# Optimization experiments

Measured on AMD Instinct MI355X. Metric: run time of the kernel, lower is better.

## Reference

```python
import jax, jax.numpy as jnp
import numpy as np
from jax import lax

B, CIN, COUT, K, H, W, SDIM = 16, 256, 256, 3, 64, 64, 512


def setup_inputs() -> dict:
    key = jax.random.key(0)
    k1, k2, k3, k4 = jax.random.split(key, 4)
    return {
        "x": jax.random.normal(k1, (B, CIN, H, W), jnp.float32),
        "style": jax.random.normal(k2, (B, SDIM), jnp.float32),
        "weight": jax.random.normal(k3, (COUT, CIN, K, K), jnp.float32),
        "style_w": jax.random.normal(k4, (SDIM, CIN), jnp.float32) * (1.0 / np.sqrt(SDIM)),
        "style_b": jnp.zeros((CIN,), jnp.float32),
    }


def reference(x, style, weight, style_w, style_b):
    b, cin, h, w_sz = x.shape
    cout, _, k, _ = weight.shape
    mod_scale = 1.0 / np.sqrt(cin * k * k)
    # style projection: [B, CIN]
    s = style @ style_w + style_b
    # modulate: [B, COUT, CIN, K, K]
    wmod = weight[None] * s[:, None, :, None, None] * mod_scale
    # demodulate over (cin, kh, kw)
    demod = lax.rsqrt(jnp.sum(wmod * wmod, axis=(2, 3, 4)) + 1e-8)  # [B, COUT]
    wmod = wmod * demod[:, :, None, None, None]
    # per-sample conv (groups=batch equivalent) via vmap
    def conv1(xb, wb):
        # xb: [CIN, H, W], wb: [COUT, CIN, K, K]
        return lax.conv_general_dilated(
            xb[None], wb, window_strides=(1, 1), padding=[(1, 1), (1, 1)],
            dimension_numbers=("NCHW", "OIHW", "NCHW"))[0]
    return jax.vmap(conv1)(x, wmod)  # [B, COUT, H, W]
```

## Files before the change

kernel.cpp:

```cpp
#include <hip/hip_runtime.h>
#include <hip/hip_bf16.h>

#define BB 16
#define CIN 256
#define COUT 256
#define HH 64
#define WW 64
#define SDIM 512

typedef __attribute__((ext_vector_type(8))) short bf16x8;
typedef __attribute__((ext_vector_type(4))) float f32x4;

static __device__ __forceinline__ short f2bf(float v) {
    __hip_bfloat16 h = __float2bfloat16(v);
    return *reinterpret_cast<short*>(&h);
}

__global__ void style_proj_kernel(const float* __restrict__ style,
                                  const float* __restrict__ style_w,
                                  const float* __restrict__ style_b,
                                  float* __restrict__ s) {
    __shared__ float red[3][64];
    int l    = threadIdx.x & 63;
    int part = threadIdx.x >> 6;
    int ci   = blockIdx.x * 64 + l;
    int b    = blockIdx.y;
    float acc = 0.f;
    const float* st = style + b * SDIM + part * (SDIM / 4);
    const float* W  = style_w + (size_t)(part * (SDIM / 4)) * CIN + ci;
#pragma unroll 4
    for (int k = 0; k < SDIM / 4; ++k) acc += st[k] * W[(size_t)k * CIN];
    if (part) red[part - 1][l] = acc;
    __syncthreads();
    if (part == 0)
        s[b * CIN + ci] = acc + red[0][l] + red[1][l] + red[2][l] + style_b[ci];
}

__global__ void wprep_kernel(const float* __restrict__ w,
                             __hip_bfloat16* __restrict__ wT,
                             float* __restrict__ wsq) {
    int co = blockIdx.x;
    int ci = threadIdx.x;
    const float* wp = w + ((size_t)co * CIN + ci) * 9;
    float acc = 0.f;
#pragma unroll
    for (int k = 0; k < 9; ++k) {
        float v = wp[k];
        acc += v * v;
        wT[((size_t)co * 9 + k) * CIN + ci] = __float2bfloat16(v);
    }
    wsq[co * CIN + ci] = acc;
}

__global__ void demod_kernel(const float* __restrict__ wsq,
                             const float* __restrict__ s,
                             float* __restrict__ demod) {
    int b    = blockIdx.y;
    int co   = blockIdx.x * 4 + (threadIdx.x >> 6);
    int lane = threadIdx.x & 63;
    float acc = 0.f;
#pragma unroll
    for (int j = 0; j < CIN / 64; ++j) {
        int ci = j * 64 + lane;
        float sv = s[b * CIN + ci];
        acc += wsq[co * CIN + ci] * sv * sv;
    }
#pragma unroll
    for (int off = 32; off > 0; off >>= 1)
        acc += __shfl_down(acc, off, 64);
    if (lane == 0)
        demod[b * COUT + co] = rsqrtf(acc * (1.0f / (CIN * 9)) + 1e-8f);
}

__global__ void xmod_kernel(const float* __restrict__ x,
                            const float* __restrict__ s,
                            __hip_bfloat16* __restrict__ xm) {
    int px = threadIdx.x & 63;
    int y  = blockIdx.x * 4 + (threadIdx.x >> 6);
    int g  = blockIdx.y;
    int b  = blockIdx.z;
    const float* xp = x + (((size_t)(b * CIN + g * 8)) * HH + y) * WW + px;
    const float4* sp = (const float4*)(s + b * CIN + g * 8);
    float4 s0 = sp[0], s1 = sp[1];
    float sv[8] = {s0.x, s0.y, s0.z, s0.w, s1.x, s1.y, s1.z, s1.w};
    bf16x8 v;
#pragma unroll
    for (int c = 0; c < 8; ++c) v[c] = f2bf(xp[(size_t)c * (HH * WW)] * sv[c]);
    *(bf16x8*)(xm + ((((size_t)(b * 32 + g)) * HH + y) * WW + px) * 8) = v;
}

__device__ __forceinline__ void stage_lds(__hip_bfloat16* xsb,
                                          const __hip_bfloat16* __restrict__ xm,
                                          int b, int cc, int Y0, int lane,
                                          int wave) {
#pragma unroll
    for (int i = 0; i < 6; ++i) {
        int u = wave * 6 + i;
        int r = u >> 2, quad = u & 3;
        int y = Y0 - 1 + r;
        if ((unsigned)y < (unsigned)HH) {
            __hip_bfloat16* dst = xsb + (((r * 4 + quad) * 66) + 1) * 8;
            const __hip_bfloat16* src =
                xm + ((((size_t)(b * 32 + cc * 4 + quad)) * HH + y) * WW + lane) * 8;
            __builtin_amdgcn_global_load_lds(
                (const __attribute__((address_space(1))) void*)src,
                (__attribute__((address_space(3))) void*)dst, 16, 0, 0);
        }
    }
}

__global__ __launch_bounds__(256, 3) void conv_mfma_kernel(
    const __hip_bfloat16* __restrict__ xm, const __hip_bfloat16* __restrict__ wT,
    const float* __restrict__ demod, float* __restrict__ out) {
    __shared__ __hip_bfloat16 xs[2][6 * 4 * 66 * 8];

    int tid  = threadIdx.x;
    int lane = tid & 63;
    int wave = tid >> 6;
    int wco  = wave >> 1;
    int rp   = wave & 1;
    int n    = lane & 15;
    int quad = lane >> 4;

    int Y0  = blockIdx.x * 4;
    int co0 = blockIdx.y * 64;
    int b   = blockIdx.z;

    const bf16x8 zv = (bf16x8){0, 0, 0, 0, 0, 0, 0, 0};
    if (tid < 96) {
        int buf = tid / 48, idx = tid % 48;
        int rowq = idx >> 1, col = (idx & 1) * 65;
        *(bf16x8*)(&xs[buf][(rowq * 66 + col) * 8]) = zv;
    }
    if (Y0 == 0) {
        for (int c = tid; c < 528; c += 256) {
            int buf = c / 264, idx = c % 264;
            *(bf16x8*)(&xs[buf][idx * 8]) = zv;
        }
    }
    if (Y0 + 4 == HH) {
        for (int c = tid; c < 528; c += 256) {
            int buf = c / 264, idx = c % 264;
            *(bf16x8*)(&xs[buf][(20 * 66 + idx) * 8]) = zv;
        }
    }

    f32x4 acc[2][2][4];
#pragma unroll
    for (int wr = 0; wr < 2; ++wr)
#pragma unroll
        for (int m = 0; m < 2; ++m)
#pragma unroll
            for (int j = 0; j < 4; ++j) acc[wr][m][j] = (f32x4){0.f, 0.f, 0.f, 0.f};

    const __hip_bfloat16* wb =
        wT + ((size_t)(co0 + wco * 32 + n) * 9) * CIN + quad * 8;

    stage_lds(xs[0], xm, b, 0, Y0, lane, wave);
    __syncthreads();

    for (int cc = 0; cc < 8; ++cc) {
        int cur = cc & 1;

        bf16x8 af[2][9];
#pragma unroll
        for (int k = 0; k < 9; ++k) {
            af[0][k] = *(const bf16x8*)(wb + ((size_t)k) * CIN + cc * 32);
            af[1][k] = *(const bf16x8*)(wb + ((size_t)(16 * 9 + k)) * CIN + cc * 32);
        }
        if (cc < 7) stage_lds(xs[cur ^ 1], xm, b, cc + 1, Y0, lane, wave);

        const __hip_bfloat16* xb = xs[cur];
#pragma unroll
        for (int r4 = 0; r4 < 4; ++r4) {
            int rr = rp * 2 + r4;
#pragma unroll
            for (int dx = 0; dx < 3; ++dx) {
#pragma unroll
                for (int j = 0; j < 4; ++j) {
                    bf16x8 bv = *(const bf16x8*)(
                        xb + (((rr * 4 + quad) * 66) + j * 16 + n + dx) * 8);
                    if (r4 <= 2) {
                        acc[0][0][j] = __builtin_amdgcn_mfma_f32_16x16x32_bf16(
                            af[0][r4 * 3 + dx], bv, acc[0][0][j], 0, 0, 0);
                        acc[0][1][j] = __builtin_amdgcn_mfma_f32_16x16x32_bf16(
                            af[1][r4 * 3 + dx], bv, acc[0][1][j], 0, 0, 0);
                    }
                    if (r4 >= 1) {
                        acc[1][0][j] = __builtin_amdgcn_mfma_f32_16x16x32_bf16(
                            af[0][(r4 - 1) * 3 + dx], bv, acc[1][0][j], 0, 0, 0);
                        acc[1][1][j] = __builtin_amdgcn_mfma_f32_16x16x32_bf16(
                            af[1][(r4 - 1) * 3 + dx], bv, acc[1][1][j], 0, 0, 0);
                    }
                }
            }
        }
        __syncthreads();
    }

    const float ms = 1.0f / 48.0f;
#pragma unroll
    for (int wr = 0; wr < 2; ++wr) {
        int gy = Y0 + rp * 2 + wr;
#pragma unroll
        for (int m = 0; m < 2; ++m) {
            int cobase = co0 + wco * 32 + m * 16 + quad * 4;
            float d0 = demod[b * COUT + cobase + 0] * ms;
            float d1 = demod[b * COUT + cobase + 1] * ms;
            float d2 = demod[b * COUT + cobase + 2] * ms;
            float d3 = demod[b * COUT + cobase + 3] * ms;
#pragma unroll
            for (int j = 0; j < 4; ++j) {
                int gx = j * 16 + n;
                size_t o = ((size_t)(b * COUT + cobase) * HH + gy) * WW + gx;
                out[o]                       = acc[wr][m][j][0] * d0;
                out[o + (size_t)HH * WW]     = acc[wr][m][j][1] * d1;
                out[o + (size_t)2 * HH * WW] = acc[wr][m][j][2] * d2;
                out[o + (size_t)3 * HH * WW] = acc[wr][m][j][3] * d3;
            }
        }
    }
}

__device__ __forceinline__ void stage_tile(
    __hip_bfloat16* __restrict__ xsb,
    const float* __restrict__ x, const float* __restrict__ s,
    int b, int cc, int Y0, int lane, int wave) {
#pragma unroll
    for (int i = 0; i < 6; ++i) {
        int u = wave * 6 + i;
        int r = u >> 2, quad = u & 3;
        int y = Y0 - 1 + r;
        bf16x8 wv = (bf16x8){0, 0, 0, 0, 0, 0, 0, 0};
        if ((unsigned)y < (unsigned)HH) {
            const float* base =
                x + (((size_t)(b * CIN + cc * 32 + quad * 8)) * HH + y) * WW + lane;
            const float4* sp = (const float4*)(s + b * CIN + cc * 32 + quad * 8);
            float4 s0 = sp[0], s1 = sp[1];
            float sv[8] = {s0.x, s0.y, s0.z, s0.w, s1.x, s1.y, s1.z, s1.w};
#pragma unroll
            for (int c = 0; c < 8; ++c)
                wv[c] = f2bf(base[(size_t)c * (HH * WW)] * sv[c]);
        }
        *(bf16x8*)(xsb + (((r * 4 + quad) * 66) + 1 + lane) * 8) = wv;
        if (lane < 2) {
            bf16x8 z = (bf16x8){0, 0, 0, 0, 0, 0, 0, 0};
            *(bf16x8*)(xsb + (((r * 4 + quad) * 66) + lane * 65) * 8) = z;
        }
    }
}

__global__ __launch_bounds__(256, 2) void conv_mfma_fb(
    const float* __restrict__ x, const __hip_bfloat16* __restrict__ wT,
    const float* __restrict__ s, const float* __restrict__ demod,
    float* __restrict__ out) {
    __shared__ __hip_bfloat16 xs[2][6 * 4 * 66 * 8];

    int tid  = threadIdx.x;
    int lane = tid & 63;
    int wave = tid >> 6;
    int wco  = wave >> 1;
    int rp   = wave & 1;
    int n    = lane & 15;
    int quad = lane >> 4;

    int Y0  = blockIdx.x * 4;
    int co0 = blockIdx.y * 64;
    int b   = blockIdx.z;

    f32x4 acc[2][2][4];
#pragma unroll
    for (int wr = 0; wr < 2; ++wr)
#pragma unroll
        for (int m = 0; m < 2; ++m)
#pragma unroll
            for (int j = 0; j < 4; ++j) acc[wr][m][j] = (f32x4){0.f, 0.f, 0.f, 0.f};

    const __hip_bfloat16* wb =
        wT + ((size_t)(co0 + wco * 32 + n) * 9) * CIN + quad * 8;

    stage_tile(xs[0], x, s, b, 0, Y0, lane, wave);
    __syncthreads();

    for (int cc = 0; cc < 8; ++cc) {
        int cur = cc & 1;
        if (cc < 7) stage_tile(xs[cur ^ 1], x, s, b, cc + 1, Y0, lane, wave);

        bf16x8 af[2][9];
#pragma unroll
        for (int k = 0; k < 9; ++k) {
            af[0][k] = *(const bf16x8*)(wb + ((size_t)k) * CIN + cc * 32);
            af[1][k] = *(const bf16x8*)(wb + ((size_t)(16 * 9 + k)) * CIN + cc * 32);
        }

        const __hip_bfloat16* xb = xs[cur];
#pragma unroll
        for (int r4 = 0; r4 < 4; ++r4) {
            int rr = rp * 2 + r4;
#pragma unroll
            for (int dx = 0; dx < 3; ++dx) {
#pragma unroll
                for (int j = 0; j < 4; ++j) {
                    bf16x8 bv = *(const bf16x8*)(
                        xb + (((rr * 4 + quad) * 66) + j * 16 + n + dx) * 8);
                    if (r4 <= 2) {
                        acc[0][0][j] = __builtin_amdgcn_mfma_f32_16x16x32_bf16(
                            af[0][r4 * 3 + dx], bv, acc[0][0][j], 0, 0, 0);
                        acc[0][1][j] = __builtin_amdgcn_mfma_f32_16x16x32_bf16(
                            af[1][r4 * 3 + dx], bv, acc[0][1][j], 0, 0, 0);
                    }
                    if (r4 >= 1) {
                        acc[1][0][j] = __builtin_amdgcn_mfma_f32_16x16x32_bf16(
                            af[0][(r4 - 1) * 3 + dx], bv, acc[1][0][j], 0, 0, 0);
                        acc[1][1][j] = __builtin_amdgcn_mfma_f32_16x16x32_bf16(
                            af[1][(r4 - 1) * 3 + dx], bv, acc[1][1][j], 0, 0, 0);
                    }
                }
            }
        }
        __syncthreads();
    }

    const float ms = 1.0f / 48.0f;
#pragma unroll
    for (int wr = 0; wr < 2; ++wr) {
        int gy = Y0 + rp * 2 + wr;
#pragma unroll
        for (int m = 0; m < 2; ++m) {
            int cobase = co0 + wco * 32 + m * 16 + quad * 4;
            float d0 = demod[b * COUT + cobase + 0] * ms;
            float d1 = demod[b * COUT + cobase + 1] * ms;
            float d2 = demod[b * COUT + cobase + 2] * ms;
            float d3 = demod[b * COUT + cobase + 3] * ms;
#pragma unroll
            for (int j = 0; j < 4; ++j) {
                int gx = j * 16 + n;
                size_t o = ((size_t)(b * COUT + cobase) * HH + gy) * WW + gx;
                out[o]                       = acc[wr][m][j][0] * d0;
                out[o + (size_t)HH * WW]     = acc[wr][m][j][1] * d1;
                out[o + (size_t)2 * HH * WW] = acc[wr][m][j][2] * d2;
                out[o + (size_t)3 * HH * WW] = acc[wr][m][j][3] * d3;
            }
        }
    }
}

extern "C" void kernel_launch(void* const* d_in, const int* in_sizes, int n_in,
                              void* d_out, int out_size, void* d_ws, size_t ws_size,
                              hipStream_t stream) {
    const float* x       = (const float*)d_in[0];
    const float* style   = (const float*)d_in[1];
    const float* weight  = (const float*)d_in[2];
    const float* style_w = (const float*)d_in[3];
    const float* style_b = (const float*)d_in[4];
    float* out = (float*)d_out;

    float* s     = (float*)d_ws;
    float* wsq   = s + BB * CIN;
    float* demod = wsq + COUT * CIN;
    __hip_bfloat16* wT = (__hip_bfloat16*)(demod + BB * COUT);
    __hip_bfloat16* xm = wT + (size_t)COUT * 9 * CIN;

    size_t need = (size_t)(BB * CIN + COUT * CIN + BB * COUT) * sizeof(float) +
                  (size_t)COUT * 9 * CIN * sizeof(__hip_bfloat16) +
                  (size_t)BB * CIN * HH * WW * sizeof(__hip_bfloat16);

    style_proj_kernel<<<dim3(CIN / 64, BB), 256, 0, stream>>>(style, style_w,
                                                              style_b, s);
    wprep_kernel<<<COUT, CIN, 0, stream>>>(weight, wT, wsq);
    demod_kernel<<<dim3(COUT / 4, BB), 256, 0, stream>>>(wsq, s, demod);

    if (ws_size >= need) {
        xmod_kernel<<<dim3(HH / 4, CIN / 8, BB), 256, 0, stream>>>(x, s, xm);
        conv_mfma_kernel<<<dim3(HH / 4, COUT / 64, BB), 256, 0, stream>>>(
            xm, wT, demod, out);
    } else {
        conv_mfma_fb<<<dim3(HH / 4, COUT / 64, BB), 256, 0, stream>>>(
            x, wT, s, demod, out);
    }
}
```

Baseline: 240.8 us.

## Single-buffer LDS with register staging, raise occupancy, fuse demod into conv

Replaces the double-buffered LDS tile filled by direct global_load_lds with a single LDS buffer, staging the next channel chunk in registers and writing it after a barrier. This halves shared memory so launch bounds can go from 3 to 4 blocks per CU. It also folds the demodulation computation into the conv kernel's prologue, removing one launch. The cost is an extra barrier per chunk, more register pressure, and redundant demod work repeated across blocks.

Result: slower. 355.2 us (+47.5%).

```diff
diff --git a/kernel.cpp b/kernel.cpp
--- a/kernel.cpp
+++ b/kernel.cpp
@@ -89,30 +89,38 @@
     *(bf16x8*)(xm + ((((size_t)(b * 32 + g)) * HH + y) * WW + px) * 8) = v;
 }
 
-__device__ __forceinline__ void stage_lds(__hip_bfloat16* xsb,
-                                          const __hip_bfloat16* __restrict__ xm,
-                                          int b, int cc, int Y0, int lane,
-                                          int wave) {
+__device__ __forceinline__ void stage_regs(bf16x8 st[6],
+                                           const __hip_bfloat16* __restrict__ xm,
+                                           int b, int cc, int Y0, int lane,
+                                           int wave) {
 #pragma unroll
     for (int i = 0; i < 6; ++i) {
         int u = wave * 6 + i;
         int r = u >> 2, quad = u & 3;
         int y = Y0 - 1 + r;
-        if ((unsigned)y < (unsigned)HH) {
-            __hip_bfloat16* dst = xsb + (((r * 4 + quad) * 66) + 1) * 8;
-            const __hip_bfloat16* src =
-                xm + ((((size_t)(b * 32 + cc * 4 + quad)) * HH + y) * WW + lane) * 8;
-            __builtin_amdgcn_global_load_lds(
-                (const __attribute__((address_space(1))) void*)src,
-                (__attribute__((address_space(3))) void*)dst, 16, 0, 0);
-        }
-    }
-}
-
-__global__ __launch_bounds__(256, 3) void conv_mfma_kernel(
+        st[i] = (bf16x8){0, 0, 0, 0, 0, 0, 0, 0};
+        if ((unsigned)y < (unsigned)HH)
+            st[i] = *(const bf16x8*)(
+                xm + ((((size_t)(b * 32 + cc * 4 + quad)) * HH + y) * WW + lane) * 8);
+    }
+}
+
+__device__ __forceinline__ void write_lds(__hip_bfloat16* xs, const bf16x8 st[6],
+                                          int lane, int wave) {
+#pragma unroll
+    for (int i = 0; i < 6; ++i) {
+        int u = wave * 6 + i;
+        int r = u >> 2, quad = u & 3;
+        *(bf16x8*)(xs + (((r * 4 + quad) * 66) + 1 + lane) * 8) = st[i];
+    }
+}
+
+__global__ __launch_bounds__(256, 4) void conv_mfma_kernel(
     const __hip_bfloat16* __restrict__ xm, const __hip_bfloat16* __restrict__ wT,
-    const float* __restrict__ demod, float* __restrict__ out) {
-    __shared__ __hip_bfloat16 xs[2][6 * 4 * 66 * 8];
+    const float* __restrict__ wsq, const float* __restrict__ s,
+    float* __restrict__ out) {
+    __shared__ __hip_bfloat16 xs[6 * 4 * 66 * 8];
+    __shared__ float dls[64];
 
     int tid  = threadIdx.x;
     int lane = tid & 63;
@@ -126,23 +134,29 @@
     int co0 = blockIdx.y * 64;
     int b   = blockIdx.z;
 
-    const bf16x8 zv = (bf16x8){0, 0, 0, 0, 0, 0, 0, 0};
-    if (tid < 96) {
-        int buf = tid / 48, idx = tid % 48;
-        int rowq = idx >> 1, col = (idx & 1) * 65;
-        *(bf16x8*)(&xs[buf][(rowq * 66 + col) * 8]) = zv;
-    }
-    if (Y0 == 0) {
-        for (int c = tid; c < 528; c += 256) {
-            int buf = c / 264, idx = c % 264;
-            *(bf16x8*)(&xs[buf][idx * 8]) = zv;
-        }
-    }
-    if (Y0 + 4 == HH) {
-        for (int c = tid; c < 528; c += 256) {
-            int buf = c / 264, idx = c % 264;
-            *(bf16x8*)(&xs[buf][(20 * 66 + idx) * 8]) = zv;
-        }
+    if (tid < 48) {
+        int rowq = tid >> 1, col = (tid & 1) * 65;
+        *(bf16x8*)(&xs[(rowq * 66 + col) * 8]) =
+            (bf16x8){0, 0, 0, 0, 0, 0, 0, 0};
+    }
+
+    bf16x8 st[6];
+    stage_regs(st, xm, b, 0, Y0, lane, wave);
+
+    {
+        int colco = tid >> 2, part = tid & 3;
+        float dacc = 0.f;
+        const float* wrow = wsq + (size_t)(co0 + colco) * CIN + part * 64;
+        const float* srow = s + b * CIN + part * 64;
+#pragma unroll 8
+        for (int i = 0; i < 64; ++i) {
+            float sv = srow[i];
+            dacc += wrow[i] * sv * sv;
+        }
+        dacc += __shfl_down(dacc, 2, 64);
+        dacc += __shfl_down(dacc, 1, 64);
+        if (part == 0)
+            dls[colco] = rsqrtf(dacc * (1.0f / (CIN * 9)) + 1e-8f);
     }
 
     f32x4 acc[2][2][4];
@@ -156,19 +170,144 @@
     const __hip_bfloat16* wb =
         wT + ((size_t)(co0 + wco * 32 + n) * 9) * CIN + quad * 8;
 
-    stage_lds(xs[0], xm, b, 0, Y0, lane, wave);
+    write_lds(xs, st, lane, wave);
     __syncthreads();
 
     for (int cc = 0; cc < 8; ++cc) {
-        int cur = cc & 1;
-
         bf16x8 af[2][9];
 #pragma unroll
         for (int k = 0; k < 9; ++k) {
             af[0][k] = *(const bf16x8*)(wb + ((size_t)k) * CIN + cc * 32);
             af[1][k] = *(const bf16x8*)(wb + ((size_t)(16 * 9 + k)) * CIN + cc * 32);
         }
-        if (cc < 7) stage_lds(xs[cur ^ 1], xm, b, cc + 1, Y0, lane, wave);
+        if (cc < 7) stage_regs(st, xm, b, cc + 1, Y0, lane, wave);
+
+#pragma unroll
+        for (int r4 = 0; r4 < 4; ++r4) {
+            int rr = rp * 2 + r4;
+#pragma unroll
+            for (int dx = 0; dx < 3; ++dx) {
+#pragma unroll
+                for (int j = 0; j < 4; ++j) {
+                    bf16x8 bv = *(const bf16x8*)(
+                        xs + (((rr * 4 + quad) * 66) + j * 16 + n + dx) * 8);
+                    if (r4 <= 2) {
+                        acc[0][0][j] = __builtin_amdgcn_mfma_f32_16x16x32_bf16(
+                            af[0][r4 * 3 + dx], bv, acc[0][0][j], 0, 0, 0);
+                        acc[0][1][j] = __builtin_amdgcn_mfma_f32_16x16x32_bf16(
+                            af[1][r4 * 3 + dx], bv, acc[0][1][j], 0, 0, 0);
+                    }
+                    if (r4 >= 1) {
+                        acc[1][0][j] = __builtin_amdgcn_mfma_f32_16x16x32_bf16(
+                            af[0][(r4 - 1) * 3 + dx], bv, acc[1][0][j], 0, 0, 0);
+                        acc[1][1][j] = __builtin_amdgcn_mfma_f32_16x16x32_bf16(
+                            af[1][(r4 - 1) * 3 + dx], bv, acc[1][1][j], 0, 0, 0);
+                    }
+                }
+            }
+        }
+        __syncthreads();
+        if (cc < 7) {
+            write_lds(xs, st, lane, wave);
+            __syncthreads();
+        }
+    }
+
+    const float ms = 1.0f / 48.0f;
+#pragma unroll
+    for (int wr = 0; wr < 2; ++wr) {
+        int gy = Y0 + rp * 2 + wr;
+#pragma unroll
+        for (int m = 0; m < 2; ++m) {
+            int cl = wco * 32 + m * 16 + quad * 4;
+            int cobase = co0 + cl;
+            float d0 = dls[cl + 0] * ms;
+            float d1 = dls[cl + 1] * ms;
+            float d2 = dls[cl + 2] * ms;
+            float d3 = dls[cl + 3] * ms;
+#pragma unroll
+            for (int j = 0; j < 4; ++j) {
+                int gx = j * 16 + n;
+                size_t o = ((size_t)(b * COUT + cobase) * HH + gy) * WW + gx;
+                out[o]                       = acc[wr][m][j][0] * d0;
+                out[o + (size_t)HH * WW]     = acc[wr][m][j][1] * d1;
+                out[o + (size_t)2 * HH * WW] = acc[wr][m][j][2] * d2;
+                out[o + (size_t)3 * HH * WW] = acc[wr][m][j][3] * d3;
+            }
+        }
+    }
+}
+
+__device__ __forceinline__ void stage_tile(
+    __hip_bfloat16* __restrict__ xsb,
+    const float* __restrict__ x, const float* __restrict__ s,
+    int b, int cc, int Y0, int lane, int wave) {
+#pragma unroll
+    for (int i = 0; i < 6; ++i) {
+        int u = wave * 6 + i;
+        int r = u >> 2, quad = u & 3;
+        int y = Y0 - 1 + r;
+        bf16x8 wv = (bf16x8){0, 0, 0, 0, 0, 0, 0, 0};
+        if ((unsigned)y < (unsigned)HH) {
+            const float* base =
+                x + (((size_t)(b * CIN + cc * 32 + quad * 8)) * HH + y) * WW + lane;
+            const float4* sp = (const float4*)(s + b * CIN + cc * 32 + quad * 8);
+            float4 s0 = sp[0], s1 = sp[1];
+            float sv[8] = {s0.x, s0.y, s0.z, s0.w, s1.x, s1.y, s1.z, s1.w};
+#pragma unroll
+            for (int c = 0; c < 8; ++c)
+                wv[c] = f2bf(base[(size_t)c * (HH * WW)] * sv[c]);
+        }
+        *(bf16x8*)(xsb + (((r * 4 + quad) * 66) + 1 + lane) * 8) = wv;
+        if (lane < 2) {
+            bf16x8 z = (bf16x8){0, 0, 0, 0, 0, 0, 0, 0};
+            *(bf16x8*)(xsb + (((r * 4 + quad) * 66) + lane * 65) * 8) = z;
+        }
+    }
+}
+
+__global__ __launch_bounds__(256, 2) void conv_mfma_fb(
+    const float* __restrict__ x, const __hip_bfloat16* __restrict__ wT,
+    const float* __restrict__ s, const float* __restrict__ demod,
+    float* __restrict__ out) {
+    __shared__ __hip_bfloat16 xs[2][6 * 4 * 66 * 8];
+
+    int tid  = threadIdx.x;
+    int lane = tid & 63;
+    int wave = tid >> 6;
+    int wco  = wave >> 1;
+    int rp   = wave & 1;
+    int n    = lane & 15;
+    int quad = lane >> 4;
+
+    int Y0  = blockIdx.x * 4;
+    int co0 = blockIdx.y * 64;
+    int b   = blockIdx.z;
+
+    f32x4 acc[2][2][4];
+#pragma unroll
+    for (int wr = 0; wr < 2; ++wr)
+#pragma unroll
+        for (int m = 0; m < 2; ++m)
+#pragma unroll
+            for (int j = 0; j < 4; ++j) acc[wr][m][j] = (f32x4){0.f, 0.f, 0.f, 0.f};
+
+    const __hip_bfloat16* wb =
+        wT + ((size_t)(co0 + wco * 32 + n) * 9) * CIN + quad * 8;
+
+    stage_tile(xs[0], x, s, b, 0, Y0, lane, wave);
+    __syncthreads();
+
+    for (int cc = 0; cc < 8; ++cc) {
+        int cur = cc & 1;
+        if (cc < 7) stage_tile(xs[cur ^ 1], x, s, b, cc + 1, Y0, lane, wave);
+
+        bf16x8 af[2][9];
+#pragma unroll
+        for (int k = 0; k < 9; ++k) {
+            af[0][k] = *(const bf16x8*)(wb + ((size_t)k) * CIN + cc * 32);
+            af[1][k] = *(const bf16x8*)(wb + ((size_t)(16 * 9 + k)) * CIN + cc * 32);
+        }
 
         const __hip_bfloat16* xb = xs[cur];
 #pragma unroll
@@ -222,129 +361,6 @@
     }
 }
 
-__device__ __forceinline__ void stage_tile(
-    __hip_bfloat16* __restrict__ xsb,
-    const float* __restrict__ x, const float* __restrict__ s,
-    int b, int cc, int Y0, int lane, int wave) {
-#pragma unroll
-    for (int i = 0; i < 6; ++i) {
-        int u = wave * 6 + i;
-        int r = u >> 2, quad = u & 3;
-        int y = Y0 - 1 + r;
-        bf16x8 wv = (bf16x8){0, 0, 0, 0, 0, 0, 0, 0};
-        if ((unsigned)y < (unsigned)HH) {
-            const float* base =
-                x + (((size_t)(b * CIN + cc * 32 + quad * 8)) * HH + y) * WW + lane;
-            const float4* sp = (const float4*)(s + b * CIN + cc * 32 + quad * 8);
-            float4 s0 = sp[0], s1 = sp[1];
-            float sv[8] = {s0.x, s0.y, s0.z, s0.w, s1.x, s1.y, s1.z, s1.w};
-#pragma unroll
-            for (int c = 0; c < 8; ++c)
-                wv[c] = f2bf(base[(size_t)c * (HH * WW)] * sv[c]);
-        }
-        *(bf16x8*)(xsb + (((r * 4 + quad) * 66) + 1 + lane) * 8) = wv;
-        if (lane < 2) {
-            bf16x8 z = (bf16x8){0, 0, 0, 0, 0, 0, 0, 0};
-            *(bf16x8*)(xsb + (((r * 4 + quad) * 66) + lane * 65) * 8) = z;
-        }
-    }
-}
-
-__global__ __launch_bounds__(256, 2) void conv_mfma_fb(
-    const float* __restrict__ x, const __hip_bfloat16* __restrict__ wT,
-    const float* __restrict__ s, const float* __restrict__ demod,
-    float* __restrict__ out) {
-    __shared__ __hip_bfloat16 xs[2][6 * 4 * 66 * 8];
-
-    int tid  = threadIdx.x;
-    int lane = tid & 63;
-    int wave = tid >> 6;
-    int wco  = wave >> 1;
-    int rp   = wave & 1;
-    int n    = lane & 15;
-    int quad = lane >> 4;
-
-    int Y0  = blockIdx.x * 4;
-    int co0 = blockIdx.y * 64;
-    int b   = blockIdx.z;
-
-    f32x4 acc[2][2][4];
-#pragma unroll
-    for (int wr = 0; wr < 2; ++wr)
-#pragma unroll
-        for (int m = 0; m < 2; ++m)
-#pragma unroll
-            for (int j = 0; j < 4; ++j) acc[wr][m][j] = (f32x4){0.f, 0.f, 0.f, 0.f};
-
-    const __hip_bfloat16* wb =
-        wT + ((size_t)(co0 + wco * 32 + n) * 9) * CIN + quad * 8;
-
-    stage_tile(xs[0], x, s, b, 0, Y0, lane, wave);
-    __syncthreads();
-
-    for (int cc = 0; cc < 8; ++cc) {
-        int cur = cc & 1;
-        if (cc < 7) stage_tile(xs[cur ^ 1], x, s, b, cc + 1, Y0, lane, wave);
-
-        bf16x8 af[2][9];
-#pragma unroll
-        for (int k = 0; k < 9; ++k) {
-            af[0][k] = *(const bf16x8*)(wb + ((size_t)k) * CIN + cc * 32);
-            af[1][k] = *(const bf16x8*)(wb + ((size_t)(16 * 9 + k)) * CIN + cc * 32);
-        }
-
-        const __hip_bfloat16* xb = xs[cur];
-#pragma unroll
-        for (int r4 = 0; r4 < 4; ++r4) {
-            int rr = rp * 2 + r4;
-#pragma unroll
-            for (int dx = 0; dx < 3; ++dx) {
-#pragma unroll
-                for (int j = 0; j < 4; ++j) {
-                    bf16x8 bv = *(const bf16x8*)(
-                        xb + (((rr * 4 + quad) * 66) + j * 16 + n + dx) * 8);
-                    if (r4 <= 2) {
-                        acc[0][0][j] = __builtin_amdgcn_mfma_f32_16x16x32_bf16(
-                            af[0][r4 * 3 + dx], bv, acc[0][0][j], 0, 0, 0);
-                        acc[0][1][j] = __builtin_amdgcn_mfma_f32_16x16x32_bf16(
-                            af[1][r4 * 3 + dx], bv, acc[0][1][j], 0, 0, 0);
-                    }
-                    if (r4 >= 1) {
-                        acc[1][0][j] = __builtin_amdgcn_mfma_f32_16x16x32_bf16(
-                            af[0][(r4 - 1) * 3 + dx], bv, acc[1][0][j], 0, 0, 0);
-                        acc[1][1][j] = __builtin_amdgcn_mfma_f32_16x16x32_bf16(
-                            af[1][(r4 - 1) * 3 + dx], bv, acc[1][1][j], 0, 0, 0);
-                    }
-                }
-            }
-        }
-        __syncthreads();
-    }
-
-    const float ms = 1.0f / 48.0f;
-#pragma unroll
-    for (int wr = 0; wr < 2; ++wr) {
-        int gy = Y0 + rp * 2 + wr;
-#pragma unroll
-        for (int m = 0; m < 2; ++m) {
-            int cobase = co0 + wco * 32 + m * 16 + quad * 4;
-            float d0 = demod[b * COUT + cobase + 0] * ms;
-            float d1 = demod[b * COUT + cobase + 1] * ms;
-            float d2 = demod[b * COUT + cobase + 2] * ms;
-            float d3 = demod[b * COUT + cobase + 3] * ms;
-#pragma unroll
-            for (int j = 0; j < 4; ++j) {
-                int gx = j * 16 + n;
-                size_t o = ((size_t)(b * COUT + cobase) * HH + gy) * WW + gx;
-                out[o]                       = acc[wr][m][j][0] * d0;
-                out[o + (size_t)HH * WW]     = acc[wr][m][j][1] * d1;
-                out[o + (size_t)2 * HH * WW] = acc[wr][m][j][2] * d2;
-                out[o + (size_t)3 * HH * WW] = acc[wr][m][j][3] * d3;
-            }
-        }
-    }
-}
-
 extern "C" void kernel_launch(void* const* d_in, const int* in_sizes, int n_in,
                               void* d_out, int out_size, void* d_ws, size_t ws_size,
                               hipStream_t stream) {
@@ -368,13 +384,13 @@
     style_proj_kernel<<<dim3(CIN / 64, BB), 256, 0, stream>>>(style, style_w,
                                                               style_b, s);
     wprep_kernel<<<COUT, CIN, 0, stream>>>(weight, wT, wsq);
-    demod_kernel<<<dim3(COUT / 4, BB), 256, 0, stream>>>(wsq, s, demod);
 
     if (ws_size >= need) {
         xmod_kernel<<<dim3(HH / 4, CIN / 8, BB), 256, 0, stream>>>(x, s, xm);
         conv_mfma_kernel<<<dim3(HH / 4, COUT / 64, BB), 256, 0, stream>>>(
-            xm, wT, demod, out);
+            xm, wT, wsq, s, out);
     } else {
+        demod_kernel<<<dim3(COUT / 4, BB), 256, 0, stream>>>(wsq, s, demod);
         conv_mfma_fb<<<dim3(HH / 4, COUT / 64, BB), 256, 0, stream>>>(
             x, wT, s, demod, out);
     }
```
